# Kernel tuning notes

Hardware: AMD Instinct MI355X
Metric: run time of the kernel (lower is better)

Reference implementation:

```python
import jax, jax.numpy as jnp
import numpy as np

B, T, F, D, NCLS = 32, 1024, 128, 64, 11
EPS = 1e-3  # keras BatchNormalization default epsilon


def sinusoidal_pe(t, f, dtype=jnp.float32):
    pos = jnp.arange(t, dtype=jnp.float32)[:, None]                      # [T,1]
    div = jnp.exp(-jnp.log(10000.0) * jnp.arange(0, f, 2, dtype=jnp.float32) / f)
    ang = pos * div                                                      # [T,F/2]
    pe = jnp.zeros((t, f), dtype=jnp.float32)
    pe = pe.at[:, 0::2].set(jnp.sin(ang)).at[:, 1::2].set(jnp.cos(ang))
    return pe.astype(dtype)


def setup_inputs() -> dict:
    key = jax.random.key(0)
    ks = jax.random.split(key, 18)
    s = 0.05
    return {
        "x": jax.random.normal(ks[0], (B, T, F), jnp.float32),
        "wq": jax.random.normal(ks[1], (F, D), jnp.float32) * s,
        "wk": jax.random.normal(ks[2], (F, D), jnp.float32) * s,
        "wv": jax.random.normal(ks[3], (F, D), jnp.float32) * s,
        "bn_a_gamma": jax.random.uniform(ks[4], (D,), jnp.float32, 0.5, 1.5),
        "bn_a_beta": jax.random.normal(ks[5], (D,), jnp.float32) * s,
        "bn_a_mean": jax.random.normal(ks[6], (D,), jnp.float32) * s,
        "bn_a_var": jax.random.uniform(ks[7], (D,), jnp.float32, 0.5, 1.5),
        "w0": jax.random.normal(ks[8], (D, 64), jnp.float32) * s,
        "b0": jax.random.normal(ks[9], (64,), jnp.float32) * s,
        "w1": jax.random.normal(ks[10], (F, 64), jnp.float32) * s,
        "b1": jax.random.normal(ks[11], (64,), jnp.float32) * s,
        "bn1_gamma": jax.random.uniform(ks[12], (128,), jnp.float32, 0.5, 1.5),
        "bn1_beta": jax.random.normal(ks[13], (128,), jnp.float32) * s,
        "bn1_mean": jax.random.normal(ks[14], (128,), jnp.float32) * s,
        "bn1_var": jax.random.uniform(ks[15], (128,), jnp.float32, 0.5, 1.5),
        "wd": jax.random.normal(ks[16], (128, NCLS), jnp.float32) * s,
        "bd": jax.random.normal(ks[17], (NCLS,), jnp.float32) * s,
    }


def _bn(h, gamma, beta, mean, var):
    # inference-mode batch norm over last axis
    return (h - mean) * (gamma * jax.lax.rsqrt(var + EPS)) + beta


def reference(x, wq, wk, wv, bn_a_gamma, bn_a_beta, bn_a_mean, bn_a_var,
              w0, b0, w1, b1, bn1_gamma, bn1_beta, bn1_mean, bn1_var, wd, bd):
    # AttentionLayer: positional encoding + single-head scaled dot-product attention
    xp = x + sinusoidal_pe(x.shape[1], x.shape[2], x.dtype)              # [B,T,F]
    q = jnp.einsum("btf,fd->btd", xp, wq)
    k = jnp.einsum("btf,fd->btd", xp, wk)
    v = jnp.einsum("btf,fd->btd", xp, wv)
    scores = jnp.einsum("bqd,bkd->bqk", q, k) / jnp.sqrt(jnp.float32(D))  # [B,T,T]
    attn = jax.nn.softmax(scores, axis=-1)
    x1 = jnp.einsum("bqk,bkd->bqd", attn, v)                             # [B,T,D]
    x1 = _bn(x1, bn_a_gamma, bn_a_beta, bn_a_mean, bn_a_var)
    # per-timestep heads (vectorized over T)
    out1 = jax.nn.relu(jnp.einsum("btd,de->bte", x1, w0) + b0)           # [B,T,64]
    out2 = jax.nn.relu(jnp.einsum("btf,fe->bte", x, w1) + b1)            # [B,T,64]
    h = jnp.concatenate([out1, out2], axis=-1)                           # [B,T,128]
    h = _bn(h, bn1_gamma, bn1_beta, bn1_mean, bn1_var)
    # dropout is identity in inference mode
    logits = jnp.einsum("bte,ec->btc", h, wd) + bd                       # [B,T,11]
    return jax.nn.softmax(logits, axis=-1)
```

## Files before the change

### kernel.cpp

```cpp
#include <hip/hip_runtime.h>
#include <math.h>

#define BB 32
#define TT 1024
#define FF 128
#define DD 64
#define NCLS 11
constexpr float kEps = 1e-3f;
constexpr int M = BB * TT;

typedef __attribute__((ext_vector_type(8))) short short8v;
typedef __attribute__((ext_vector_type(4))) short short4v;
typedef __attribute__((ext_vector_type(4))) float float4v;
typedef __attribute__((ext_vector_type(16))) float float16v;

__device__ __forceinline__ short f2bf(float f) {
  union { float f; unsigned u; } v; v.f = f;
  return (short)((v.u + 0x7FFFu + ((v.u >> 16) & 1u)) >> 16);
}
__device__ __forceinline__ float bf2f(short s) {
  union { unsigned u; float f; } v; v.u = ((unsigned)(unsigned short)s) << 16;
  return v.f;
}

__device__ __forceinline__ short8v pack_swap(
    float p0, float p1, float p2, float p3,
    float p4, float p5, float p6, float p7) {
  unsigned a0, a1, b0, b1;
  asm("v_cvt_pk_bf16_f32 %0, %1, %2" : "=v"(a0) : "v"(p0), "v"(p1));
  asm("v_cvt_pk_bf16_f32 %0, %1, %2" : "=v"(a1) : "v"(p2), "v"(p3));
  asm("v_cvt_pk_bf16_f32 %0, %1, %2" : "=v"(b0) : "v"(p4), "v"(p5));
  asm("v_cvt_pk_bf16_f32 %0, %1, %2" : "=v"(b1) : "v"(p6), "v"(p7));
  asm volatile("v_permlane32_swap_b32 %0, %1" : "+v"(a0), "+v"(b0));
  asm volatile("v_permlane32_swap_b32 %0, %1" : "+v"(a1), "+v"(b1));
  union { unsigned u[4]; short8v s; } r;
  r.u[0] = a0; r.u[1] = a1; r.u[2] = b0; r.u[3] = b1;
  return r.s;
}

__global__ __launch_bounds__(256) void prep_kernel(
    const float* __restrict__ wq, const float* __restrict__ wk,
    const float* __restrict__ wv, const float* __restrict__ w1,
    const float* __restrict__ w0, const float* __restrict__ b0,
    const float* __restrict__ bn_a_gamma, const float* __restrict__ bn_a_beta,
    const float* __restrict__ bn_a_mean, const float* __restrict__ bn_a_var,
    const float* __restrict__ bn1_gamma, const float* __restrict__ bn1_beta,
    const float* __restrict__ bn1_mean, const float* __restrict__ bn1_var,
    const float* __restrict__ wd, const float* __restrict__ bd,
    short* __restrict__ wT4,
    short* __restrict__ w0pT, float* __restrict__ b0p,
    short* __restrict__ wdpT, float* __restrict__ bdp,
    float* __restrict__ peq, float* __restrict__ pek, float* __restrict__ pev) {
  const int t = threadIdx.x;
  const int blk = blockIdx.x;

  if (blk >= 5) {
    __shared__ float peL[16][128];
    const int p = blk - 5;
    const int y = p >> 6;
    const int t0 = (p & 63) * 16;
#pragma unroll
    for (int i = 0; i < 8; ++i) {
      const int idx = t + i * 256;
      const int tr = idx >> 7, f = idx & 127;
      const float div = expf(-logf(10000.0f) * (float)(f & ~1) / (float)FF);
      const float ang = (float)(t0 + tr) * div;
      peL[tr][f] = (f & 1) ? cosf(ang) : sinf(ang);
    }
    __syncthreads();
    const float* w = (y == 0) ? wq : (y == 1) ? wk : wv;
    float* dst = (y == 0) ? peq : (y == 1) ? pek : pev;
    const int tr = t >> 4, dq = t & 15;
    float4 acc = {0.f, 0.f, 0.f, 0.f};
    for (int f = 0; f < FF; ++f) {
      const float pv = peL[tr][f];
      const float4 w4 = *(const float4*)&w[f * 64 + dq * 4];
      acc.x += pv * w4.x; acc.y += pv * w4.y;
      acc.z += pv * w4.z; acc.w += pv * w4.w;
    }
    *(float4*)&dst[(t0 + tr) * 64 + dq * 4] = acc;
    return;
  }
  if (blk > 0) {
    const int y = blk - 1;
    const float* w = (y == 0) ? wq : (y == 1) ? wk : (y == 2) ? wv : w1;
    short* dst = wT4 + y * 8192;
#pragma unroll
    for (int i = 0; i < 4; ++i) {
      const int idx = t + i * 256;
      const int n = idx >> 4, c = idx & 15;
      short8v s8;
#pragma unroll
      for (int j = 0; j < 8; ++j) s8[j] = f2bf(w[(c * 8 + j) * 64 + n]);
      *(short8v*)&dst[n * 128 + ((c ^ (n & 7)) << 3)] = s8;
    }
    return;
  }
  __shared__ float cA[64], cAo[64], c1s[64], c1o[64], c2s[64], c2o[64];
  if (t < 64) {
    const float sA = bn_a_gamma[t] * rsqrtf(bn_a_var[t] + kEps);
    cA[t] = sA; cAo[t] = bn_a_beta[t] - bn_a_mean[t] * sA;
    const float s1 = bn1_gamma[t] * rsqrtf(bn1_var[t] + kEps);
    c1s[t] = s1; c1o[t] = bn1_beta[t] - bn1_mean[t] * s1;
    const float s2 = bn1_gamma[t + 64] * rsqrtf(bn1_var[t + 64] + kEps);
    c2s[t] = s2; c2o[t] = bn1_beta[t + 64] - bn1_mean[t + 64] * s2;
  }
  __syncthreads();
  for (int i = t; i < 4096; i += 256) {
    const int e = i >> 6, k = i & 63;
    w0pT[i] = f2bf(cA[k] * w0[k * 64 + e]);
  }
  if (t < 64) {
    float s = b0[t];
    for (int k = 0; k < 64; ++k) s += cAo[k] * w0[k * 64 + t];
    b0p[t] = s;
  }
  for (int i = t; i < 2048; i += 256) {
    const int c = i >> 7, e = i & 127;
    float v = 0.f;
    if (c < NCLS) v = wd[e * NCLS + c] * (e < 64 ? c1s[e] : c2s[e - 64]);
    wdpT[i] = f2bf(v);
  }
  if (t < 16) {
    float s = 0.f;
    if (t < NCLS) {
      s = bd[t];
      for (int e = 0; e < 64; ++e) s += c1o[e] * wd[e * NCLS + t];
      for (int e = 0; e < 64; ++e) s += c2o[e] * wd[(64 + e) * NCLS + t];
    }
    bdp[t] = s;
  }
}

__global__ __launch_bounds__(256) void proj_kernel(
    const float* __restrict__ x, const short* __restrict__ wT4,
    const float* __restrict__ peq, const float* __restrict__ pek,
    const float* __restrict__ pev, const float* __restrict__ b1,
    short* __restrict__ qo, short* __restrict__ ko,
    short* __restrict__ vt, short* __restrict__ o2) {
  __shared__ __align__(16) short xs[128 * 128];
  __shared__ __align__(16) short wsh[64 * 128];
  const int tid = threadIdx.x;
  const int lane = tid & 63;
  const int wv4 = tid >> 6;
  const int l15 = lane & 15;
  const int lg = lane >> 4;
  const int r0 = blockIdx.x * 128;
  const int y = blockIdx.y;

#pragma unroll
  for (int i = 0; i < 8; ++i) {
    int id = tid + i * 256;
    int row = id >> 4, chunk = id & 15;
    const float* xp = &x[((size_t)(r0 + row)) * FF + chunk * 8];
    const float4 a = *(const float4*)xp;
    const float4 b = *(const float4*)(xp + 4);
    short8v s8;
    s8[0] = f2bf(a.x); s8[1] = f2bf(a.y); s8[2] = f2bf(a.z); s8[3] = f2bf(a.w);
    s8[4] = f2bf(b.x); s8[5] = f2bf(b.y); s8[6] = f2bf(b.z); s8[7] = f2bf(b.w);
    *(short8v*)&xs[row * 128 + ((chunk ^ (row & 7)) << 3)] = s8;
  }
#pragma unroll
  for (int i = 0; i < 4; ++i) {
    const int idx = tid + i * 256;
    *(int4*)&wsh[idx * 8] = *(const int4*)&wT4[y * 8192 + idx * 8];
  }
  __syncthreads();

  float4v acc[2][4];
#pragma unroll
  for (int rt = 0; rt < 2; ++rt)
#pragma unroll
    for (int dt = 0; dt < 4; ++dt) acc[rt][dt] = (float4v)0.0f;

  const bool natural = (y == 2);
#pragma unroll
  for (int kt = 0; kt < 4; ++kt) {
    const int chunk = kt * 4 + lg;
    short8v xa[2], wa[4];
#pragma unroll
    for (int rt = 0; rt < 2; ++rt) {
      const int row = wv4 * 32 + rt * 16 + l15;
      xa[rt] = *(const short8v*)&xs[row * 128 + ((chunk ^ (row & 7)) << 3)];
    }
#pragma unroll
    for (int dt = 0; dt < 4; ++dt) {
      const int n = dt * 16 + l15;
      wa[dt] = *(const short8v*)&wsh[n * 128 + ((chunk ^ (n & 7)) << 3)];
    }
#pragma unroll
    for (int rt = 0; rt < 2; ++rt)
#pragma unroll
      for (int dt = 0; dt < 4; ++dt)
        acc[rt][dt] = natural
            ? __builtin_amdgcn_mfma_f32_16x16x32_bf16(xa[rt], wa[dt], acc[rt][dt], 0, 0, 0)
            : __builtin_amdgcn_mfma_f32_16x16x32_bf16(wa[dt], xa[rt], acc[rt][dt], 0, 0, 0);
  }

  if (natural) {
    const int bq = r0 >> 10;
    const int tb = (r0 & 1023) + wv4 * 32;
#pragma unroll
    for (int rt = 0; rt < 2; ++rt) {
#pragma unroll
      for (int dt = 0; dt < 4; ++dt) {
        const int d = dt * 16 + l15;
        const int t0 = tb + rt * 16 + lg * 4;
        short4v s;
#pragma unroll
        for (int r = 0; r < 4; ++r)
          s[r] = f2bf(acc[rt][dt][r] + pev[(t0 + r) * 64 + d]);
        *(short4v*)&vt[((size_t)(bq * DD + d)) * TT + t0] = s;
      }
    }
  } else {
    short* dst = (y == 0) ? qo : (y == 1) ? ko : o2;
    const float* petab = (y == 0) ? peq : pek;
    const float qs = (y == 0) ? 0.18033688f : 1.0f;
#pragma unroll
    for (int rt = 0; rt < 2; ++rt) {
      const int row = r0 + wv4 * 32 + rt * 16 + l15;
      const int tr = row & 1023;
#pragma unroll
      for (int dt = 0; dt < 4; ++dt) {
        const int d0 = dt * 16 + lg * 4;
        float v0 = acc[rt][dt][0], v1 = acc[rt][dt][1];
        float v2 = acc[rt][dt][2], v3 = acc[rt][dt][3];
        if (y == 3) {
          const float4 bv = *(const float4*)&b1[d0];
          v0 = fmaxf(v0 + bv.x, 0.f); v1 = fmaxf(v1 + bv.y, 0.f);
          v2 = fmaxf(v2 + bv.z, 0.f); v3 = fmaxf(v3 + bv.w, 0.f);
        } else {
          const float4 pv = *(const float4*)&petab[tr * 64 + d0];
          v0 = (v0 + pv.x) * qs; v1 = (v1 + pv.y) * qs;
          v2 = (v2 + pv.z) * qs; v3 = (v3 + pv.w) * qs;
        }
        short4v s;
        s[0] = f2bf(v0); s[1] = f2bf(v1); s[2] = f2bf(v2); s[3] = f2bf(v3);
        *(short4v*)&dst[(size_t)row * DD + d0] = s;
      }
    }
  }
}

__global__ __launch_bounds__(256, 2) void attn_head_kernel(
    const short* __restrict__ qg, const short* __restrict__ kg,
    const short* __restrict__ vtg, const short* __restrict__ o2m,
    const short* __restrict__ w0pT, const float* __restrict__ b0p,
    const short* __restrict__ wdpT, const float* __restrict__ bdp,
    float* __restrict__ out) {
  __shared__ __align__(16) short Ks[2][2][4096];
  __shared__ __align__(16) short Vs[2][2][4096];
  const int tid = threadIdx.x;
  const int lane = tid & 63;
  const int wid = tid >> 6;
  const int qwv = wid & 1;
  const int grp = wid >> 1;
  const int id = blockIdx.x;
  const int bb = id & 31;
  const int qx = id >> 5;
  const int l31 = lane & 31;
  const int lhi = lane >> 5;
  const int l15 = lane & 15;
  const int lg = lane >> 4;
  const int qbase = qx * 64 + qwv * 32;
  const int kt0 = grp * 8;
  const int stid = tid & 127;
  const int kkey = (l31 & 7) << 3;

  short8v qf[4];
#pragma unroll
  for (int dc = 0; dc < 4; ++dc)
    qf[dc] = *(const short8v*)&qg[((size_t)(bb * TT + qbase + l31)) * DD + dc * 16 + lhi * 8];

  float16v oacc[2];
  oacc[0] = (float16v)0.f; oacc[1] = (float16v)0.f;
  float lacc = 0.f;

#pragma unroll
  for (int j = 0; j < 4; ++j) {
    const int idx = stid + j * 128;
    const int row = idx >> 3, c8 = (idx & 7) * 8;
    const int sw = c8 ^ ((row & 7) << 3);
    *(int4*)&Ks[grp][0][row * 64 + sw] =
        *(const int4*)&kg[((size_t)(bb * TT + kt0 * 64 + row)) * DD + c8];
    *(int4*)&Vs[grp][0][row * 64 + sw] =
        *(const int4*)&vtg[((size_t)(bb * DD + row)) * TT + kt0 * 64 + c8];
  }
  __syncthreads();

  for (int i = 0; i < 8; ++i) {
    const int cur = i & 1;
    int4 nk[4], nv[4];
    if (i < 7) {
      const int nt = (kt0 + i + 1) * 64;
#pragma unroll
      for (int j = 0; j < 4; ++j) {
        const int idx = stid + j * 128;
        const int row = idx >> 3, c8 = (idx & 7) * 8;
        nk[j] = *(const int4*)&kg[((size_t)(bb * TT + nt + row)) * DD + c8];
        nv[j] = *(const int4*)&vtg[((size_t)(bb * DD + row)) * TT + nt + c8];
      }
    }

    float16v s0 = (float16v)0.f, s1 = (float16v)0.f;
    {
      short8v kf[4];
#pragma unroll
      for (int dc = 0; dc < 4; ++dc)
        kf[dc] = *(const short8v*)&Ks[grp][cur][l31 * 64 + ((dc * 16 + lhi * 8) ^ kkey)];
#pragma unroll
      for (int dc = 0; dc < 4; ++dc)
        s0 = __builtin_amdgcn_mfma_f32_32x32x16_bf16(kf[dc], qf[dc], s0, 0, 0, 0);
#pragma unroll
      for (int dc = 0; dc < 4; ++dc)
        kf[dc] = *(const short8v*)&Ks[grp][cur][(32 + l31) * 64 + ((dc * 16 + lhi * 8) ^ kkey)];
#pragma unroll
      for (int dc = 0; dc < 4; ++dc)
        s1 = __builtin_amdgcn_mfma_f32_32x32x16_bf16(kf[dc], qf[dc], s1, 0, 0, 0);
    }

    float16v p0, p1;
#pragma unroll
    for (int r = 0; r < 16; ++r) { p0[r] = exp2f(s0[r]); lacc += p0[r]; }
#pragma unroll
    for (int r = 0; r < 16; ++r) { p1[r] = exp2f(s1[r]); lacc += p1[r]; }

    const short8v pfa = pack_swap(p0[0], p0[1], p0[2], p0[3], p0[4], p0[5], p0[6], p0[7]);
    const short8v pfb = pack_swap(p0[8], p0[9], p0[10], p0[11], p0[12], p0[13], p0[14], p0[15]);
    const short8v pfc = pack_swap(p1[0], p1[1], p1[2], p1[3], p1[4], p1[5], p1[6], p1[7]);
    const short8v pfd = pack_swap(p1[8], p1[9], p1[10], p1[11], p1[12], p1[13], p1[14], p1[15]);

#pragma unroll
    for (int dh = 0; dh < 2; ++dh) {
      const int drow = dh * 32 + l31;
      short8v vf[4];
#pragma unroll
      for (int c = 0; c < 4; ++c)
        vf[c] = *(const short8v*)&Vs[grp][cur][drow * 64 + ((c * 16 + lhi * 8) ^ kkey)];
      oacc[dh] = __builtin_amdgcn_mfma_f32_32x32x16_bf16(pfa, vf[0], oacc[dh], 0, 0, 0);
      oacc[dh] = __builtin_amdgcn_mfma_f32_32x32x16_bf16(pfb, vf[1], oacc[dh], 0, 0, 0);
      oacc[dh] = __builtin_amdgcn_mfma_f32_32x32x16_bf16(pfc, vf[2], oacc[dh], 0, 0, 0);
      oacc[dh] = __builtin_amdgcn_mfma_f32_32x32x16_bf16(pfd, vf[3], oacc[dh], 0, 0, 0);
    }

    if (i < 7) {
#pragma unroll
      for (int j = 0; j < 4; ++j) {
        const int idx = stid + j * 128;
        const int row = idx >> 3, c8 = (idx & 7) * 8;
        const int sw = c8 ^ ((row & 7) << 3);
        *(int4*)&Ks[grp][cur ^ 1][row * 64 + sw] = nk[j];
        *(int4*)&Vs[grp][cur ^ 1][row * 64 + sw] = nv[j];
      }
      __syncthreads();
    }
  }

  lacc += __shfl_xor(lacc, 32);

  __syncthreads();
  float* cb = (float*)&Ks[0][0][0];
  float* lcb = (float*)&Vs[1][0][0];
  if (grp == 1) {
#pragma unroll
    for (int dh = 0; dh < 2; ++dh)
#pragma unroll
      for (int r = 0; r < 16; ++r)
        cb[qwv * 2048 + (dh * 16 + r) * 64 + lane] = oacc[dh][r];
    if (lane < 32) lcb[qwv * 32 + lane] = lacc;
  }
  __syncthreads();
  if (grp == 0) {
#pragma unroll
    for (int dh = 0; dh < 2; ++dh)
#pragma unroll
      for (int r = 0; r < 16; ++r)
        oacc[dh][r] += cb[qwv * 2048 + (dh * 16 + r) * 64 + lane];
    lacc += lcb[qwv * 32 + l31];
    const float linv = 1.0f / lacc;

    short* hs = (short*)&Vs[0][0][0] + qwv * 2048;
#pragma unroll
    for (int dh = 0; dh < 2; ++dh)
#pragma unroll
      for (int r = 0; r < 16; ++r) {
        const int q = (r & 3) + 8 * (r >> 2) + 4 * lhi;
        const int d = dh * 32 + l31;
        const int chunk = d >> 3;
        hs[q * 64 + ((chunk ^ (q & 7)) << 3) + (l31 & 7)] = f2bf(oacc[dh][r]);
      }

#pragma unroll
    for (int sub = 0; sub < 2; ++sub) {
      short* hsub = hs + sub * 16 * 64;
      short8v af[2];
#pragma unroll
      for (int dt = 0; dt < 2; ++dt) {
        const int chunk = (dt * 4 + lg) ^ (l15 & 7);
        af[dt] = *(const short8v*)&hsub[l15 * 64 + chunk * 8];
      }

      float4v acc1[4];
#pragma unroll
      for (int et = 0; et < 4; ++et) acc1[et] = (float4v)0.0f;
#pragma unroll
      for (int et = 0; et < 4; ++et)
#pragma unroll
        for (int dt = 0; dt < 2; ++dt) {
          const short8v wb = *(const short8v*)&w0pT[(et * 16 + l15) * 64 + dt * 32 + lg * 8];
          acc1[et] = __builtin_amdgcn_mfma_f32_16x16x32_bf16(af[dt], wb, acc1[et], 0, 0, 0);
        }

      float b0v[4];
#pragma unroll
      for (int et = 0; et < 4; ++et) b0v[et] = b0p[et * 16 + l15];

#pragma unroll
      for (int r = 0; r < 4; ++r) {
        const float invm = __shfl(linv, sub * 16 + lg * 4 + r);
        const int m = lg * 4 + r;
#pragma unroll
        for (int et = 0; et < 4; ++et) {
          const float v = fmaxf(acc1[et][r] * invm + b0v[et], 0.f);
          const int chunk = (et * 2 + (l15 >> 3)) ^ (m & 7);
          hsub[m * 64 + chunk * 8 + (l15 & 7)] = f2bf(v);
        }
      }

      float4v accL = (float4v)0.0f;
#pragma unroll
      for (int dt = 0; dt < 2; ++dt) {
        const int chunk = (dt * 4 + lg) ^ (l15 & 7);
        const short8v ha = *(const short8v*)&hsub[l15 * 64 + chunk * 8];
        const short8v wb = *(const short8v*)&wdpT[l15 * 128 + dt * 32 + lg * 8];
        accL = __builtin_amdgcn_mfma_f32_16x16x32_bf16(ha, wb, accL, 0, 0, 0);
      }
      const size_t o2row = ((size_t)bb * TT + qbase + sub * 16 + l15) * DD;
#pragma unroll
      for (int dt = 0; dt < 2; ++dt) {
        const short8v ha = *(const short8v*)&o2m[o2row + dt * 32 + lg * 8];
        const short8v wb = *(const short8v*)&wdpT[l15 * 128 + 64 + dt * 32 + lg * 8];
        accL = __builtin_amdgcn_mfma_f32_16x16x32_bf16(ha, wb, accL, 0, 0, 0);
      }

      const float bdv = bdp[l15];
#pragma unroll
      for (int r = 0; r < 4; ++r) {
        const float lv = (l15 < NCLS) ? (accL[r] + bdv) : -1e30f;
        float mx = lv;
#pragma unroll
        for (int off = 1; off < 16; off <<= 1) mx = fmaxf(mx, __shfl_xor(mx, off));
        const float ex = (l15 < NCLS) ? __expf(lv - mx) : 0.f;
        float sm = ex;
#pragma unroll
        for (int off = 1; off < 16; off <<= 1) sm += __shfl_xor(sm, off);
        if (l15 < NCLS)
          out[((size_t)bb * TT + qbase + sub * 16 + lg * 4 + r) * NCLS + l15] = ex / sm;
      }
    }
  }
}

extern "C" void kernel_launch(void* const* d_in, const int* in_sizes, int n_in,
                              void* d_out, int out_size, void* d_ws, size_t ws_size,
                              hipStream_t stream) {
  (void)in_sizes; (void)n_in; (void)out_size; (void)ws_size;
  const float* x  = (const float*)d_in[0];
  const float* wq = (const float*)d_in[1];
  const float* wk = (const float*)d_in[2];
  const float* wv = (const float*)d_in[3];
  const float* bn_a_gamma = (const float*)d_in[4];
  const float* bn_a_beta  = (const float*)d_in[5];
  const float* bn_a_mean  = (const float*)d_in[6];
  const float* bn_a_var   = (const float*)d_in[7];
  const float* w0 = (const float*)d_in[8];
  const float* b0 = (const float*)d_in[9];
  const float* w1 = (const float*)d_in[10];
  const float* b1 = (const float*)d_in[11];
  const float* bn1_gamma = (const float*)d_in[12];
  const float* bn1_beta  = (const float*)d_in[13];
  const float* bn1_mean  = (const float*)d_in[14];
  const float* bn1_var   = (const float*)d_in[15];
  const float* wd = (const float*)d_in[16];
  const float* bd = (const float*)d_in[17];
  float* out = (float*)d_out;

  char* cur = (char*)d_ws;
  short* q  = (short*)cur; cur += (size_t)M * DD * 2;
  short* k  = (short*)cur; cur += (size_t)M * DD * 2;
  short* vt = (short*)cur; cur += (size_t)M * DD * 2;
  short* o2 = (short*)cur; cur += (size_t)M * DD * 2;
  short* wT4  = (short*)cur; cur += 4 * 8192 * 2;
  short* w0pT = (short*)cur; cur += 4096 * 2;
  short* wdpT = (short*)cur; cur += 2048 * 2;
  float* b0p  = (float*)cur; cur += 64 * 4;
  float* bdp  = (float*)cur; cur += 16 * 4;
  float* peq  = (float*)cur; cur += (size_t)TT * DD * 4;
  float* pek  = (float*)cur; cur += (size_t)TT * DD * 4;
  float* pev  = (float*)cur; cur += (size_t)TT * DD * 4;

  prep_kernel<<<dim3(197), dim3(256), 0, stream>>>(
      wq, wk, wv, w1, w0, b0, bn_a_gamma, bn_a_beta, bn_a_mean, bn_a_var,
      bn1_gamma, bn1_beta, bn1_mean, bn1_var, wd, bd,
      wT4, w0pT, b0p, wdpT, bdp, peq, pek, pev);
  proj_kernel<<<dim3(M / 128, 4), dim3(256), 0, stream>>>(
      x, wT4, peq, pek, pev, b1, q, k, vt, o2);
  attn_head_kernel<<<dim3(512), dim3(256), 0, stream>>>(
      q, k, vt, o2, w0pT, b0p, wdpT, bdp, out);
}
```

Baseline: 52.60 us.

## Split attention KV range across four wave groups with 512-thread blocks

```diff
diff --git a/kernel.cpp b/kernel.cpp
--- a/kernel.cpp
+++ b/kernel.cpp
@@ -243,14 +243,13 @@
   }
 }
 
-__global__ __launch_bounds__(256, 2) void attn_head_kernel(
+__global__ __launch_bounds__(512, 4) void attn_head_kernel(
     const short* __restrict__ qg, const short* __restrict__ kg,
     const short* __restrict__ vtg, const short* __restrict__ o2m,
     const short* __restrict__ w0pT, const float* __restrict__ b0p,
     const short* __restrict__ wdpT, const float* __restrict__ bdp,
     float* __restrict__ out) {
-  __shared__ __align__(16) short Ks[2][2][4096];
-  __shared__ __align__(16) short Vs[2][2][4096];
+  __shared__ __align__(16) char LB[65536];
   const int tid = threadIdx.x;
   const int lane = tid & 63;
   const int wid = tid >> 6;
@@ -264,9 +263,22 @@
   const int l15 = lane & 15;
   const int lg = lane >> 4;
   const int qbase = qx * 64 + qwv * 32;
-  const int kt0 = grp * 8;
+  const int kvbase = grp * 256;
   const int stid = tid & 127;
-  const int kkey = (l31 & 7) << 3;
+
+  short* const Kb[2] = {(short*)(LB + grp * 16384),
+                        (short*)(LB + grp * 16384 + 4096)};
+  short* const Vb[2] = {(short*)(LB + grp * 16384 + 8192),
+                        (short*)(LB + grp * 16384 + 12288)};
+
+  const int krow0 = stid >> 3, kc8 = (stid & 7) * 8;
+  const int ksw0 = kc8 ^ ((krow0 & 7) << 3);
+  const int krow1 = krow0 + 16;
+  const int ksw1 = kc8 ^ ((krow1 & 7) << 3);
+  const int vd0 = stid >> 2, vt4 = stid & 3;
+  const int vsw0 = (vt4 ^ (vd0 & 3)) * 8;
+  const int vd1 = vd0 + 32;
+  const int vsw1 = (vt4 ^ (vd1 & 3)) * 8;
 
   short8v qf[4];
 #pragma unroll
@@ -277,82 +289,68 @@
   oacc[0] = (float16v)0.f; oacc[1] = (float16v)0.f;
   float lacc = 0.f;
 
-#pragma unroll
-  for (int j = 0; j < 4; ++j) {
-    const int idx = stid + j * 128;
-    const int row = idx >> 3, c8 = (idx & 7) * 8;
-    const int sw = c8 ^ ((row & 7) << 3);
-    *(int4*)&Ks[grp][0][row * 64 + sw] =
-        *(const int4*)&kg[((size_t)(bb * TT + kt0 * 64 + row)) * DD + c8];
-    *(int4*)&Vs[grp][0][row * 64 + sw] =
-        *(const int4*)&vtg[((size_t)(bb * DD + row)) * TT + kt0 * 64 + c8];
+  {
+    *(int4*)&Kb[0][krow0 * 64 + ksw0] =
+        *(const int4*)&kg[((size_t)(bb * TT + kvbase + krow0)) * DD + kc8];
+    *(int4*)&Kb[0][krow1 * 64 + ksw1] =
+        *(const int4*)&kg[((size_t)(bb * TT + kvbase + krow1)) * DD + kc8];
+    *(int4*)&Vb[0][vd0 * 32 + vsw0] =
+        *(const int4*)&vtg[((size_t)(bb * DD + vd0)) * TT + kvbase + vt4 * 8];
+    *(int4*)&Vb[0][vd1 * 32 + vsw1] =
+        *(const int4*)&vtg[((size_t)(bb * DD + vd1)) * TT + kvbase + vt4 * 8];
   }
   __syncthreads();
 
   for (int i = 0; i < 8; ++i) {
     const int cur = i & 1;
-    int4 nk[4], nv[4];
+    short* const Kc = Kb[cur];
+    short* const Vc = Vb[cur];
+
+    int4 nk0, nk1, nv0, nv1;
     if (i < 7) {
-      const int nt = (kt0 + i + 1) * 64;
-#pragma unroll
-      for (int j = 0; j < 4; ++j) {
-        const int idx = stid + j * 128;
-        const int row = idx >> 3, c8 = (idx & 7) * 8;
-        nk[j] = *(const int4*)&kg[((size_t)(bb * TT + nt + row)) * DD + c8];
-        nv[j] = *(const int4*)&vtg[((size_t)(bb * DD + row)) * TT + nt + c8];
-      }
-    }
-
-    float16v s0 = (float16v)0.f, s1 = (float16v)0.f;
-    {
-      short8v kf[4];
-#pragma unroll
-      for (int dc = 0; dc < 4; ++dc)
-        kf[dc] = *(const short8v*)&Ks[grp][cur][l31 * 64 + ((dc * 16 + lhi * 8) ^ kkey)];
-#pragma unroll
-      for (int dc = 0; dc < 4; ++dc)
-        s0 = __builtin_amdgcn_mfma_f32_32x32x16_bf16(kf[dc], qf[dc], s0, 0, 0, 0);
-#pragma unroll
-      for (int dc = 0; dc < 4; ++dc)
-        kf[dc] = *(const short8v*)&Ks[grp][cur][(32 + l31) * 64 + ((dc * 16 + lhi * 8) ^ kkey)];
-#pragma unroll
-      for (int dc = 0; dc < 4; ++dc)
-        s1 = __builtin_amdgcn_mfma_f32_32x32x16_bf16(kf[dc], qf[dc], s1, 0, 0, 0);
-    }
-
-    float16v p0, p1;
-#pragma unroll
-    for (int r = 0; r < 16; ++r) { p0[r] = exp2f(s0[r]); lacc += p0[r]; }
-#pragma unroll
-    for (int r = 0; r < 16; ++r) { p1[r] = exp2f(s1[r]); lacc += p1[r]; }
-
-    const short8v pfa = pack_swap(p0[0], p0[1], p0[2], p0[3], p0[4], p0[5], p0[6], p0[7]);
-    const short8v pfb = pack_swap(p0[8], p0[9], p0[10], p0[11], p0[12], p0[13], p0[14], p0[15]);
-    const short8v pfc = pack_swap(p1[0], p1[1], p1[2], p1[3], p1[4], p1[5], p1[6], p1[7]);
-    const short8v pfd = pack_swap(p1[8], p1[9], p1[10], p1[11], p1[12], p1[13], p1[14], p1[15]);
+      const int nkv = kvbase + (i + 1) * 32;
+      nk0 = *(const int4*)&kg[((size_t)(bb * TT + nkv + krow0)) * DD + kc8];
+      nk1 = *(const int4*)&kg[((size_t)(bb * TT + nkv + krow1)) * DD + kc8];
+      nv0 = *(const int4*)&vtg[((size_t)(bb * DD + vd0)) * TT + nkv + vt4 * 8];
+      nv1 = *(const int4*)&vtg[((size_t)(bb * DD + vd1)) * TT + nkv + vt4 * 8];
+    }
+
+    short8v kf[4];
+#pragma unroll
+    for (int dc = 0; dc < 4; ++dc) {
+      const int chunk = (dc * 2 + lhi) ^ (l31 & 7);
+      kf[dc] = *(const short8v*)&Kc[l31 * 64 + chunk * 8];
+    }
+    float16v s = (float16v)0.f;
+#pragma unroll
+    for (int dc = 0; dc < 4; ++dc)
+      s = __builtin_amdgcn_mfma_f32_32x32x16_bf16(kf[dc], qf[dc], s, 0, 0, 0);
+
+    float16v p;
+#pragma unroll
+    for (int r = 0; r < 16; ++r) { p[r] = exp2f(s[r]); lacc += p[r]; }
+
+    const short8v pfa = pack_swap(p[0], p[1], p[2], p[3], p[4], p[5], p[6], p[7]);
+    const short8v pfb = pack_swap(p[8], p[9], p[10], p[11], p[12], p[13], p[14], p[15]);
 
 #pragma unroll
     for (int dh = 0; dh < 2; ++dh) {
       const int drow = dh * 32 + l31;
-      short8v vf[4];
-#pragma unroll
-      for (int c = 0; c < 4; ++c)
-        vf[c] = *(const short8v*)&Vs[grp][cur][drow * 64 + ((c * 16 + lhi * 8) ^ kkey)];
-      oacc[dh] = __builtin_amdgcn_mfma_f32_32x32x16_bf16(pfa, vf[0], oacc[dh], 0, 0, 0);
-      oacc[dh] = __builtin_amdgcn_mfma_f32_32x32x16_bf16(pfb, vf[1], oacc[dh], 0, 0, 0);
-      oacc[dh] = __builtin_amdgcn_mfma_f32_32x32x16_bf16(pfc, vf[2], oacc[dh], 0, 0, 0);
-      oacc[dh] = __builtin_amdgcn_mfma_f32_32x32x16_bf16(pfd, vf[3], oacc[dh], 0, 0, 0);
+      const int c0 = (lhi) ^ (drow & 3);
+      const int c1 = (2 + lhi) ^ (drow & 3);
+      const short8v vf0 = *(const short8v*)&Vc[drow * 32 + c0 * 8];
+      const short8v vf1 = *(const short8v*)&Vc[drow * 32 + c1 * 8];
+      oacc[dh] = __builtin_amdgcn_mfma_f32_32x32x16_bf16(pfa, vf0, oacc[dh], 0, 0, 0);
+      oacc[dh] = __builtin_amdgcn_mfma_f32_32x32x16_bf16(pfb, vf1, oacc[dh], 0, 0, 0);
     }
 
     if (i < 7) {
-#pragma unroll
-      for (int j = 0; j < 4; ++j) {
-        const int idx = stid + j * 128;
-        const int row = idx >> 3, c8 = (idx & 7) * 8;
-        const int sw = c8 ^ ((row & 7) << 3);
-        *(int4*)&Ks[grp][cur ^ 1][row * 64 + sw] = nk[j];
-        *(int4*)&Vs[grp][cur ^ 1][row * 64 + sw] = nv[j];
-      }
+      short* const Kn = Kb[cur ^ 1];
+      short* const Vn = Vb[cur ^ 1];
+      *(int4*)&Kn[krow0 * 64 + ksw0] = nk0;
+      *(int4*)&Kn[krow1 * 64 + ksw1] = nk1;
+      *(int4*)&Vn[vd0 * 32 + vsw0] = nv0;
+      *(int4*)&Vn[vd1 * 32 + vsw1] = nv1;
       __syncthreads();
     }
   }
@@ -360,27 +358,37 @@
   lacc += __shfl_xor(lacc, 32);
 
   __syncthreads();
-  float* cb = (float*)&Ks[0][0][0];
-  float* lcb = (float*)&Vs[1][0][0];
-  if (grp == 1) {
+  if (grp > 0) {
+    float* cb = (float*)(LB + (grp - 1) * 16384);
 #pragma unroll
     for (int dh = 0; dh < 2; ++dh)
 #pragma unroll
-      for (int r = 0; r < 16; ++r)
-        cb[qwv * 2048 + (dh * 16 + r) * 64 + lane] = oacc[dh][r];
-    if (lane < 32) lcb[qwv * 32 + lane] = lacc;
+      for (int r = 0; r < 16; ++r) {
+        const int q = (r & 3) + 8 * (r >> 2) + 4 * lhi;
+        cb[qwv * 2048 + q * 64 + dh * 32 + l31] = oacc[dh][r];
+      }
+    float* lcb = (float*)(LB + 49152);
+    if (lhi == 0) lcb[(grp - 1) * 64 + qwv * 32 + l31] = lacc;
   }
   __syncthreads();
   if (grp == 0) {
 #pragma unroll
-    for (int dh = 0; dh < 2; ++dh)
-#pragma unroll
-      for (int r = 0; r < 16; ++r)
-        oacc[dh][r] += cb[qwv * 2048 + (dh * 16 + r) * 64 + lane];
-    lacc += lcb[qwv * 32 + l31];
+    for (int g = 1; g < 4; ++g) {
+      const float* cb = (const float*)(LB + (g - 1) * 16384);
+#pragma unroll
+      for (int dh = 0; dh < 2; ++dh)
+#pragma unroll
+        for (int r = 0; r < 16; ++r) {
+          const int q = (r & 3) + 8 * (r >> 2) + 4 * lhi;
+          oacc[dh][r] += cb[qwv * 2048 + q * 64 + dh * 32 + l31];
+        }
+    }
+    const float* lcb = (const float*)(LB + 49152);
+#pragma unroll
+    for (int g = 1; g < 4; ++g) lacc += lcb[(g - 1) * 64 + qwv * 32 + l31];
     const float linv = 1.0f / lacc;
 
-    short* hs = (short*)&Vs[0][0][0] + qwv * 2048;
+    short* hs = (short*)(LB + 50176 + qwv * 4096);
 #pragma unroll
     for (int dh = 0; dh < 2; ++dh)
 #pragma unroll
@@ -506,6 +514,6 @@
       wT4, w0pT, b0p, wdpT, bdp, peq, pek, pev);
   proj_kernel<<<dim3(M / 128, 4), dim3(256), 0, stream>>>(
       x, wT4, peq, pek, pev, b1, q, k, vt, o2);
-  attn_head_kernel<<<dim3(512), dim3(256), 0, stream>>>(
+  attn_head_kernel<<<dim3(512), dim3(512), 0, stream>>>(
       q, k, vt, o2, w0pT, b0p, wdpT, bdp, out);
 }
```

Measured after the change: 54.51 us. +3.6%, slower.
